# Kernel tuning notes

Hardware: AMD Instinct MI355X
Metric: run time of the kernel (lower is better)

## Reference

```python
import jax, jax.numpy as jnp
import numpy as np

EPS = 1e-5

def rms_norm(x, scale, eps=EPS):
    rms = jax.lax.rsqrt(jnp.mean(x * x, axis=-1, keepdims=True) + eps)
    return scale * (x * rms)

def act_quant(x, min_scale=0.001, max_scale=1000.0):
    # int8 activation quantization (STE in torch; fwd math only here)
    max_val = jnp.max(jnp.abs(x), axis=-1, keepdims=True)
    s = jnp.clip(127.0 / (max_val + 1e-5), min_scale, max_scale)
    return jnp.clip(jnp.round(s * x), -128.0, 127.0) / s

def weight_quant(w, num_bits=8):
    qmax = 2.0 ** (num_bits - 1) - 1.0
    scale = qmax / (jnp.max(jnp.abs(w)) + 1e-5)
    return jnp.round(jnp.clip(w * scale, -(qmax + 1.0), qmax)) / scale

def ternarize(w):
    sf = jnp.clip(1.0 / (jnp.mean(jnp.abs(w)) + 1e-5), 1e-4, 1e4)
    return jnp.sign(w * sf)

def setup_inputs() -> dict:
    key = jax.random.key(0)
    ks = jax.random.split(key, 5)
    B, S, E, H = 8, 512, 2048, 2048
    x = jax.random.normal(ks[0], (B, S, E), dtype=jnp.float32)
    # ternary {-1,0,1} init as in ternary_initialize
    def tern_init(k, shape):
        r = jax.random.uniform(k, shape, dtype=jnp.float32)
        return jnp.where(r < 1.0 / 3.0, -1.0, jnp.where(r > 2.0 / 3.0, 1.0, 0.0))
    return {
        "x": x,
        "rms_scale": jnp.ones((H,), jnp.float32),
        "W_f": tern_init(ks[1], (E, H)),
        "W_c": tern_init(ks[2], (E, H)),
        "W_g": tern_init(ks[3], (H, E)),
        "b_f": jnp.ones((H,), jnp.float32),
        "b_c": jnp.zeros((H,), jnp.float32),
        "b_g": jnp.zeros((H,), jnp.float32),
    }

def reference(x, rms_scale, W_f, W_c, W_g, b_f, b_c, b_g):
    B, S, E = x.shape
    H = W_f.shape[1]
    # quantize + ternarize weights once (identical every timestep)
    Wt_f = ternarize(weight_quant(W_f))
    Wt_c = ternarize(weight_quant(W_c))
    Wt_g = ternarize(weight_quant(W_g))  # (H, E) but E == H

    def step(h, x_t):
        xq = act_quant(rms_norm(x_t, rms_scale))
        # matmul-free linear: x @ (pos_mask - neg_mask) == x @ sign(W)
        f_t = jax.nn.sigmoid(xq @ Wt_f + b_f)
        c_t = jax.nn.silu(xq @ Wt_c + b_c)
        g_t = jax.nn.sigmoid(xq @ Wt_g + b_g)
        h_new = f_t * h + (1.0 - f_t) * c_t
        o_t = g_t * h_new
        # layer-level copy gate: sigmoid(W_g @ x_t^T)^T = sigmoid(x_t @ W_g^T), raw weights
        cg = jax.nn.sigmoid(x_t @ W_g.T)
        h_out = cg * x_t + (1.0 - cg) * h_new
        return h_out, o_t

    h0 = jnp.zeros((B, H), x.dtype)
    _, outs = jax.lax.scan(step, h0, jnp.swapaxes(x, 0, 1))  # scan over S
    return jnp.swapaxes(outs, 0, 1)  # (B, S, H)
```

## Files before the change

kernel.cpp:

```cpp
#include <hip/hip_runtime.h>
#include <hip/hip_bf16.h>
#include <cstdint>
#include <cstddef>

#define RTOT 4096
#define DIM  2048
#define NCAT 6144
#define NCHUNK 16
#define TCHUNK 32

typedef __attribute__((ext_vector_type(4))) int int4v;

__device__ __forceinline__ float fast_sigmoid(float z) {
    return __builtin_amdgcn_rcpf(1.0f + __expf(-z));
}
__device__ __forceinline__ unsigned short f2h(float f) {
    union { _Float16 h; unsigned short u; } v; v.h = (_Float16)f; return v.u;
}
__device__ __forceinline__ float h2f(unsigned short u) {
    union { _Float16 h; unsigned short u; } v; v.u = u; return (float)v.h;
}

#define GLDS(gp, lp) __builtin_amdgcn_global_load_lds( \
    (__attribute__((address_space(1))) const void*)(gp), \
    (__attribute__((address_space(3))) void*)(lp), 16, 0, 0)

__device__ __forceinline__ int4v frag_ld(const signed char* lds, int R, int lq) {
    return *(const int4v*)(lds + R * 64 + ((lq ^ ((R >> 1) & 3)) * 16));
}

__global__ __launch_bounds__(256) void prep_all(
    const float* __restrict__ x, const float* __restrict__ scale,
    const float* __restrict__ Wf, const float* __restrict__ Wc,
    const float* __restrict__ Wg,
    signed char* __restrict__ WcatT, signed char* __restrict__ Wgb,
    signed char* __restrict__ Xq, signed char* __restrict__ Q1,
    signed char* __restrict__ Q2, float* __restrict__ s_arr,
    float* __restrict__ s1_arr)
{
    __shared__ __align__(16) char smem[4224];
    int bid = blockIdx.x;
    int tid = threadIdx.x;
    if (bid < 3072) {
        signed char (*tile)[65] = (signed char(*)[65])smem;
        int j0 = (bid % 96) * 64;
        int k0 = (bid / 96) * 64;
        const float* W = (j0 < 2048) ? Wf : (j0 < 4096) ? Wc : Wg;
        int jb = j0 & 2047;
        int c  = tid & 63;
        int rr = tid >> 6;
#pragma unroll
        for (int p = 0; p < 16; ++p) {
            int kl = p * 4 + rr;
            tile[kl][c] = (signed char)(int)W[(size_t)(k0 + kl) * DIM + jb + c];
        }
        __syncthreads();
#pragma unroll
        for (int p = 0; p < 16; ++p) {
            int jl = p * 4 + rr;
            WcatT[(size_t)(j0 + jl) * DIM + k0 + c] = tile[c][jl];
        }
    } else if (bid < 4096) {
        int idx = (bid - 3072) * 4096 + tid * 16;
#pragma unroll
        for (int p = 0; p < 4; ++p) {
            float4 v = *(const float4*)(Wg + idx + p * 4);
            char4 o;
            o.x = (signed char)(int)v.x; o.y = (signed char)(int)v.y;
            o.z = (signed char)(int)v.z; o.w = (signed char)(int)v.w;
            *(char4*)(Wgb + idx + p * 4) = o;
        }
    } else {
        float* red = (float*)smem;
        float* tot = (float*)(smem + 64);
        int row = bid - 4096;
        const float* xr = x + (size_t)row * DIM + tid * 8;
        const float* sr = scale + tid * 8;
        float4 a0 = *(const float4*)(xr);
        float4 a1 = *(const float4*)(xr + 4);
        float4 c0 = *(const float4*)(sr);
        float4 c1 = *(const float4*)(sr + 4);
        float xs[8] = {a0.x, a0.y, a0.z, a0.w, a1.x, a1.y, a1.z, a1.w};
        float sc[8] = {c0.x, c0.y, c0.z, c0.w, c1.x, c1.y, c1.z, c1.w};
        float sum = 0.f, mx2 = 0.f;
#pragma unroll
        for (int i = 0; i < 8; ++i) {
            sum += xs[i] * xs[i];
            mx2 = fmaxf(mx2, fabsf(xs[i]));
        }
#pragma unroll
        for (int off = 32; off > 0; off >>= 1) {
            sum += __shfl_down(sum, off);
            mx2 = fmaxf(mx2, __shfl_down(mx2, off));
        }
        int lane = tid & 63, wv = tid >> 6;
        if (lane == 0) { red[wv] = sum; red[4 + wv] = mx2; }
        __syncthreads();
        if (tid == 0) {
            tot[0] = red[0] + red[1] + red[2] + red[3];
            tot[1] = fmaxf(fmaxf(red[4], red[5]), fmaxf(red[6], red[7]));
        }
        __syncthreads();
        float rms = 1.0f / sqrtf(tot[0] * (1.0f / 2048.0f) + 1e-5f);
        float y[8]; float mx = 0.f;
#pragma unroll
        for (int i = 0; i < 8; ++i) {
            y[i] = (xs[i] * rms) * sc[i];
            mx = fmaxf(mx, fabsf(y[i]));
        }
#pragma unroll
        for (int off = 32; off > 0; off >>= 1) mx = fmaxf(mx, __shfl_down(mx, off));
        if (lane == 0) red[8 + wv] = mx;
        __syncthreads();
        if (tid == 0)
            tot[2] = fmaxf(fmaxf(red[8], red[9]), fmaxf(red[10], red[11]));
        __syncthreads();
        float s = 127.0f / (tot[2] + 1e-5f);
        s = fminf(fmaxf(s, 0.001f), 1000.0f);
        float s1 = 127.0f / (tot[1] + 1e-5f);
        float inv_s1 = 1.0f / s1;
        if (tid == 0) { s_arr[row] = s; s1_arr[row] = s1; }
        signed char q8[8], q1b[8], q2b[8];
#pragma unroll
        for (int i = 0; i < 8; ++i) {
            float q = fminf(fmaxf(rintf(s * y[i]), -128.f), 127.f);
            q8[i] = (signed char)(int)q;
            float qq1 = fminf(fmaxf(rintf(s1 * xs[i]), -128.f), 127.f);
            q1b[i] = (signed char)(int)qq1;
            float r = xs[i] - qq1 * inv_s1;
            float qq2 = fminf(fmaxf(rintf(s1 * 256.f * r), -128.f), 127.f);
            q2b[i] = (signed char)(int)qq2;
        }
        size_t o = (size_t)row * DIM + tid * 8;
        *(int2*)(Xq + o) = *(int2*)q8;
        *(int2*)(Q1 + o) = *(int2*)q1b;
        *(int2*)(Q2 + o) = *(int2*)q2b;
    }
}

__global__ __launch_bounds__(256) void gemm_all(
    const signed char* __restrict__ Xq, const signed char* __restrict__ WcatT,
    const signed char* __restrict__ Q1, const signed char* __restrict__ Q2,
    const signed char* __restrict__ Wgb,
    const float* __restrict__ s_arr, const float* __restrict__ s1_arr,
    const float* __restrict__ b_f, const float* __restrict__ b_c,
    const float* __restrict__ b_g,
    unsigned short* __restrict__ FCG,
    unsigned short* __restrict__ U,
    unsigned short* __restrict__ V)
{
    __shared__ __align__(16) signed char lds[32768];
    int bid = blockIdx.x;
    int grp = bid / 5, r5 = bid % 5;
    int tid = threadIdx.x;
    int lane = tid & 63, wv = tid >> 6;
    int lr = lane & 15, lq = lane >> 4;
    int rA = lane >> 2;
    int gch = ((lane & 3) ^ ((lane >> 3) & 3)) * 16;

    if (r5 < 3) {
        int fb = grp * 3 + r5;
        int m0 = (fb / 48) * 128;
        int n0 = (fb % 48) * 128;
        int wm = (wv >> 1) * 64, wn = (wv & 1) * 64;
        const signed char* Ab = Xq + (size_t)m0 * DIM;
        const signed char* Bb = WcatT + (size_t)n0 * DIM;

        int4v acc[4][4] = {};
#pragma unroll
        for (int it = 0; it < 2; ++it) {
            int region = wv + it * 4;
            int rr = region * 16 + rA;
            GLDS(Ab + (size_t)rr * DIM + gch, lds + region * 1024);
            GLDS(Bb + (size_t)rr * DIM + gch, lds + 8192 + region * 1024);
        }
        for (int k6 = 0; k6 < 32; ++k6) {
            signed char* cur = lds + (k6 & 1) * 16384;
            signed char* nxt = lds + ((k6 + 1) & 1) * 16384;
            __syncthreads();
            if (k6 + 1 < 32) {
                int kt = (k6 + 1) * 64;
#pragma unroll
                for (int it = 0; it < 2; ++it) {
                    int region = wv + it * 4;
                    int rr = region * 16 + rA;
                    GLDS(Ab + (size_t)rr * DIM + kt + gch, nxt + region * 1024);
                    GLDS(Bb + (size_t)rr * DIM + kt + gch, nxt + 8192 + region * 1024);
                }
            }
            int4v af[4], bb[4];
#pragma unroll
            for (int i = 0; i < 4; ++i) af[i] = frag_ld(cur, wm + i * 16 + lr, lq);
#pragma unroll
            for (int j = 0; j < 4; ++j) bb[j] = frag_ld(cur + 8192, wn + j * 16 + lr, lq);
#pragma unroll
            for (int i = 0; i < 4; ++i)
#pragma unroll
                for (int j = 0; j < 4; ++j)
                    acc[i][j] = __builtin_amdgcn_mfma_i32_16x16x64_i8(
                        af[i], bb[j], acc[i][j], 0, 0, 0);
        }
#pragma unroll
        for (int i = 0; i < 4; ++i) {
            float rinv[4];
#pragma unroll
            for (int r = 0; r < 4; ++r)
                rinv[r] = __builtin_amdgcn_rcpf(s_arr[m0 + wm + i * 16 + lq * 4 + r]);
#pragma unroll
            for (int j = 0; j < 4; ++j) {
                int gcol = n0 + wn + j * 16 + lr;
                int sec = gcol >> 11;
                int jj = gcol & 2047;
                float bias = (sec == 0) ? b_f[jj] : (sec == 1) ? b_c[jj] : b_g[jj];
#pragma unroll
                for (int r = 0; r < 4; ++r) {
                    int grow = m0 + wm + i * 16 + lq * 4 + r;
                    float z = fmaf((float)acc[i][j][r], rinv[r], bias);
                    float sg = fast_sigmoid(z);
                    FCG[(size_t)grow * NCAT + gcol] = f2h((sec == 1) ? z * sg : sg);
                }
            }
        }
    } else {
        int cb = grp * 2 + (r5 - 3);
        int m0 = (cb >> 4) * 64;
        int n0 = (cb & 15) * 128;
        int wm = (wv >> 1) * 32, wn = (wv & 1) * 64;
        const signed char* A1b = Q1 + (size_t)m0 * DIM;
        const signed char* A2b = Q2 + (size_t)m0 * DIM;
        const signed char* Bb  = Wgb + (size_t)n0 * DIM;
        int r1 = wv * 16 + rA;

        int4v acc1[2][4] = {};
        int4v acc2[2][4] = {};
        {
            GLDS(A1b + (size_t)r1 * DIM + gch, lds + wv * 1024);
            GLDS(A2b + (size_t)r1 * DIM + gch, lds + 4096 + wv * 1024);
#pragma unroll
            for (int it = 0; it < 2; ++it) {
                int region = wv + it * 4;
                int rr = region * 16 + rA;
                GLDS(Bb + (size_t)rr * DIM + gch, lds + 8192 + region * 1024);
            }
        }
        for (int k6 = 0; k6 < 32; ++k6) {
            signed char* cur = lds + (k6 & 1) * 16384;
            signed char* nxt = lds + ((k6 + 1) & 1) * 16384;
            __syncthreads();
            if (k6 + 1 < 32) {
                int kt = (k6 + 1) * 64;
                GLDS(A1b + (size_t)r1 * DIM + kt + gch, nxt + wv * 1024);
                GLDS(A2b + (size_t)r1 * DIM + kt + gch, nxt + 4096 + wv * 1024);
#pragma unroll
                for (int it = 0; it < 2; ++it) {
                    int region = wv + it * 4;
                    int rr = region * 16 + rA;
                    GLDS(Bb + (size_t)rr * DIM + kt + gch, nxt + 8192 + region * 1024);
                }
            }
            int4v bb[4];
#pragma unroll
            for (int j = 0; j < 4; ++j) bb[j] = frag_ld(cur + 8192, wn + j * 16 + lr, lq);
#pragma unroll
            for (int i = 0; i < 2; ++i) {
                int4v a1 = frag_ld(cur, wm + i * 16 + lr, lq);
                int4v a2 = frag_ld(cur + 4096, wm + i * 16 + lr, lq);
#pragma unroll
                for (int j = 0; j < 4; ++j) {
                    acc1[i][j] = __builtin_amdgcn_mfma_i32_16x16x64_i8(
                        a1, bb[j], acc1[i][j], 0, 0, 0);
                    acc2[i][j] = __builtin_amdgcn_mfma_i32_16x16x64_i8(
                        a2, bb[j], acc2[i][j], 0, 0, 0);
                }
            }
        }
#pragma unroll
        for (int i = 0; i < 2; ++i) {
            float rinv[4];
#pragma unroll
            for (int r = 0; r < 4; ++r)
                rinv[r] = __builtin_amdgcn_rcpf(s1_arr[m0 + wm + i * 16 + lq * 4 + r]);
#pragma unroll
            for (int j = 0; j < 4; ++j) {
                int gcol = n0 + wn + j * 16 + lr;
#pragma unroll
                for (int r = 0; r < 4; ++r) {
                    int grow = m0 + wm + i * 16 + lq * 4 + r;
                    size_t go = (size_t)grow * DIM + gcol;
                    float zs = (float)acc1[i][j][r] + (float)acc2[i][j][r] * (1.f / 256.f);
                    float cg = fast_sigmoid(zs * rinv[r]);
                    float xv = ((float)Q1[go] + (float)Q2[go] * (1.f / 256.f)) * rinv[r];
                    U[go] = f2h(cg * xv);
                    V[go] = f2h(1.f - cg);
                }
            }
        }
    }
}

__global__ __launch_bounds__(256) void scan_partial(
    const unsigned short* __restrict__ FCG, const unsigned short* __restrict__ U,
    const unsigned short* __restrict__ V, float4* __restrict__ PQ4)
{
    int tp = blockIdx.x * 256 + threadIdx.x;
    int c = blockIdx.y;
    int b = blockIdx.z;
    int h0 = tp * 2;
    size_t r0 = (size_t)(b * 512 + c * TCHUNK);
    const unsigned short* fp = FCG + r0 * NCAT + h0;
    const unsigned short* up = U + r0 * DIM + h0;
    const unsigned short* vp = V + r0 * DIM + h0;
    float P0 = 1.f, Q0 = 0.f, P1 = 1.f, Q1v = 0.f;
#pragma unroll 4
    for (int t = 0; t < TCHUNK; ++t) {
        unsigned fw = *(const unsigned*)(fp);
        unsigned cw = *(const unsigned*)(fp + 2048);
        unsigned uw = *(const unsigned*)(up);
        unsigned vw = *(const unsigned*)(vp);
        float f0 = h2f(fw & 0xffff), f1 = h2f(fw >> 16);
        float c0 = h2f(cw & 0xffff), c1 = h2f(cw >> 16);
        float u0 = h2f(uw & 0xffff), u1 = h2f(uw >> 16);
        float v0 = h2f(vw & 0xffff), v1 = h2f(vw >> 16);
        float A0 = v0 * f0, A1 = v1 * f1;
        float B0 = fmaf(v0 * (1.f - f0), c0, u0);
        float B1 = fmaf(v1 * (1.f - f1), c1, u1);
        P0 = A0 * P0; Q0 = fmaf(A0, Q0, B0);
        P1 = A1 * P1; Q1v = fmaf(A1, Q1v, B1);
        fp += NCAT; up += DIM; vp += DIM;
    }
    float4 o; o.x = P0; o.y = Q0; o.z = P1; o.w = Q1v;
    PQ4[(size_t)c * 8192 + b * 1024 + tp] = o;
}

__global__ __launch_bounds__(256) void scan_final(
    const unsigned short* __restrict__ FCG, const unsigned short* __restrict__ U,
    const unsigned short* __restrict__ V, const float4* __restrict__ PQ4,
    float* __restrict__ out)
{
    int tp = blockIdx.x * 256 + threadIdx.x;
    int c = blockIdx.y;
    int b = blockIdx.z;
    int h0 = tp * 2;
    float h0s = 0.f, h1s = 0.f;
    for (int cc = 0; cc < c; ++cc) {
        float4 pq = PQ4[(size_t)cc * 8192 + b * 1024 + tp];
        h0s = fmaf(pq.x, h0s, pq.y);
        h1s = fmaf(pq.z, h1s, pq.w);
    }
    size_t r0 = (size_t)(b * 512 + c * TCHUNK);
    const unsigned short* fp = FCG + r0 * NCAT + h0;
    const unsigned short* up = U + r0 * DIM + h0;
    const unsigned short* vp = V + r0 * DIM + h0;
    float* op = out + r0 * DIM + h0;
#pragma unroll 4
    for (int t = 0; t < TCHUNK; ++t) {
        unsigned fw = *(const unsigned*)(fp);
        unsigned cw = *(const unsigned*)(fp + 2048);
        unsigned gw = *(const unsigned*)(fp + 4096);
        unsigned uw = *(const unsigned*)(up);
        unsigned vw = *(const unsigned*)(vp);
        float f0 = h2f(fw & 0xffff), f1 = h2f(fw >> 16);
        float c0 = h2f(cw & 0xffff), c1 = h2f(cw >> 16);
        float g0 = h2f(gw & 0xffff), g1 = h2f(gw >> 16);
        float u0 = h2f(uw & 0xffff), u1 = h2f(uw >> 16);
        float v0 = h2f(vw & 0xffff), v1 = h2f(vw >> 16);
        float hn0 = f0 * h0s + (1.f - f0) * c0;
        float hn1 = f1 * h1s + (1.f - f1) * c1;
        float2 ov; ov.x = g0 * hn0; ov.y = g1 * hn1;
        *(float2*)op = ov;
        h0s = fmaf(v0, hn0, u0);
        h1s = fmaf(v1, hn1, u1);
        fp += NCAT; up += DIM; vp += DIM; op += DIM;
    }
}

extern "C" void kernel_launch(void* const* d_in, const int* in_sizes, int n_in,
                              void* d_out, int out_size, void* d_ws, size_t ws_size,
                              hipStream_t stream) {
    const float* x     = (const float*)d_in[0];
    const float* rmssc = (const float*)d_in[1];
    const float* W_f   = (const float*)d_in[2];
    const float* W_c   = (const float*)d_in[3];
    const float* W_g   = (const float*)d_in[4];
    const float* b_f   = (const float*)d_in[5];
    const float* b_c   = (const float*)d_in[6];
    const float* b_g   = (const float*)d_in[7];
    float* out = (float*)d_out;

    char* ws = (char*)d_ws;
    size_t off = 0;
    auto alloc = [&](size_t bytes) -> void* {
        void* p = ws + off;
        off += (bytes + 255) & ~(size_t)255;
        return p;
    };
    signed char* WcatT = (signed char*)alloc((size_t)NCAT * DIM);
    signed char* Wgb   = (signed char*)alloc((size_t)DIM * DIM);
    signed char* Xq    = (signed char*)alloc((size_t)RTOT * DIM);
    signed char* Q1    = (signed char*)alloc((size_t)RTOT * DIM);
    signed char* Q2    = (signed char*)alloc((size_t)RTOT * DIM);
    float* s_arr       = (float*)alloc((size_t)RTOT * 4);
    float* s1_arr      = (float*)alloc((size_t)RTOT * 4);
    unsigned short* FCG = (unsigned short*)alloc((size_t)RTOT * NCAT * 2);
    unsigned short* U   = (unsigned short*)alloc((size_t)RTOT * DIM * 2);
    unsigned short* V   = (unsigned short*)alloc((size_t)RTOT * DIM * 2);
    float4* PQ4        = (float4*)alloc((size_t)NCHUNK * 8192 * 16);

    hipLaunchKernelGGL(prep_all, dim3(8192), dim3(256), 0, stream,
                       x, rmssc, W_f, W_c, W_g, WcatT, Wgb, Xq, Q1, Q2,
                       s_arr, s1_arr);
    hipLaunchKernelGGL(gemm_all, dim3(2560), dim3(256), 0, stream,
                       Xq, WcatT, Q1, Q2, Wgb, s_arr, s1_arr,
                       b_f, b_c, b_g, FCG, U, V);
    hipLaunchKernelGGL(scan_partial, dim3(DIM / 512, NCHUNK, 8), dim3(256), 0, stream,
                       FCG, U, V, PQ4);
    hipLaunchKernelGGL(scan_final, dim3(DIM / 512, NCHUNK, 8), dim3(256), 0, stream,
                       FCG, U, V, PQ4, out);
}
```

Before: 297.3 us.

## Split GEMMs and precompute scan coefficients in the f/c/g GEMM epilogue

Splits the combined GEMM into a copy-gate GEMM that writes packed (u,v) pairs and an f/c/g GEMM whose three waves each compute one gate for the same 64x64 tile. The f/c/g epilogue exchanges the gate values through LDS and emits precomputed scan coefficients (A,B) and output coefficients (g*f, g*(1-f)*c). The scans then read one or two packed words per step instead of five fp16 streams, and chunks are halved to 16 steps with 32 chunks. This cuts scan memory traffic and FCG intermediate size. In exchange the GEMM runs with 192 threads, adds an extra kernel launch, and scan_final's serial prefix over PQ4 gets longer.

```diff
diff --git a/kernel.cpp b/kernel.cpp
--- a/kernel.cpp
+++ b/kernel.cpp
@@ -6,8 +6,8 @@
 #define RTOT 4096
 #define DIM  2048
 #define NCAT 6144
-#define NCHUNK 16
-#define TCHUNK 32
+#define NCHUNK 32
+#define TCHUNK 16
 
 typedef __attribute__((ext_vector_type(4))) int int4v;
 
@@ -19,6 +19,9 @@
 }
 __device__ __forceinline__ float h2f(unsigned short u) {
     union { _Float16 h; unsigned short u; } v; v.u = u; return (float)v.h;
+}
+__device__ __forceinline__ unsigned pack2(float a, float b) {
+    return (unsigned)f2h(a) | ((unsigned)f2h(b) << 16);
 }
 
 #define GLDS(gp, lp) __builtin_amdgcn_global_load_lds( \
@@ -138,209 +141,206 @@
     }
 }
 
-__global__ __launch_bounds__(256) void gemm_all(
+__global__ __launch_bounds__(256) void gemm_cg(
+    const signed char* __restrict__ Q1, const signed char* __restrict__ Q2,
+    const signed char* __restrict__ Wgb, const float* __restrict__ s1_arr,
+    unsigned* __restrict__ UV)
+{
+    __shared__ __align__(16) signed char lds[32768];
+    int cb = blockIdx.x;
+    int m0 = (cb >> 4) * 64;
+    int n0 = (cb & 15) * 128;
+    int tid = threadIdx.x;
+    int lane = tid & 63, wv = tid >> 6;
+    int wm = (wv >> 1) * 32, wn = (wv & 1) * 64;
+    int lr = lane & 15, lq = lane >> 4;
+    int rA = lane >> 2;
+    int gch = ((lane & 3) ^ ((lane >> 3) & 3)) * 16;
+    const signed char* A1b = Q1 + (size_t)m0 * DIM;
+    const signed char* A2b = Q2 + (size_t)m0 * DIM;
+    const signed char* Bb  = Wgb + (size_t)n0 * DIM;
+    int r1 = wv * 16 + rA;
+
+    int4v acc1[2][4] = {};
+    int4v acc2[2][4] = {};
+    {
+        GLDS(A1b + (size_t)r1 * DIM + gch, lds + wv * 1024);
+        GLDS(A2b + (size_t)r1 * DIM + gch, lds + 4096 + wv * 1024);
+#pragma unroll
+        for (int it = 0; it < 2; ++it) {
+            int region = wv + it * 4;
+            GLDS(Bb + (size_t)(region * 16 + rA) * DIM + gch,
+                 lds + 8192 + region * 1024);
+        }
+    }
+    for (int k6 = 0; k6 < 32; ++k6) {
+        const signed char* cur = lds + (k6 & 1) * 16384;
+        signed char* nxt = lds + ((k6 + 1) & 1) * 16384;
+        __syncthreads();
+        if (k6 + 1 < 32) {
+            int kt = (k6 + 1) * 64;
+            GLDS(A1b + (size_t)r1 * DIM + kt + gch, nxt + wv * 1024);
+            GLDS(A2b + (size_t)r1 * DIM + kt + gch, nxt + 4096 + wv * 1024);
+#pragma unroll
+            for (int it = 0; it < 2; ++it) {
+                int region = wv + it * 4;
+                GLDS(Bb + (size_t)(region * 16 + rA) * DIM + kt + gch,
+                     nxt + 8192 + region * 1024);
+            }
+        }
+        int4v bb[4];
+#pragma unroll
+        for (int j = 0; j < 4; ++j) bb[j] = frag_ld(cur + 8192, wn + j * 16 + lr, lq);
+#pragma unroll
+        for (int i = 0; i < 2; ++i) {
+            int4v a1 = frag_ld(cur, wm + i * 16 + lr, lq);
+            int4v a2 = frag_ld(cur + 4096, wm + i * 16 + lr, lq);
+#pragma unroll
+            for (int j = 0; j < 4; ++j) {
+                acc1[i][j] = __builtin_amdgcn_mfma_i32_16x16x64_i8(
+                    a1, bb[j], acc1[i][j], 0, 0, 0);
+                acc2[i][j] = __builtin_amdgcn_mfma_i32_16x16x64_i8(
+                    a2, bb[j], acc2[i][j], 0, 0, 0);
+            }
+        }
+    }
+#pragma unroll
+    for (int i = 0; i < 2; ++i) {
+        float rinv[4];
+#pragma unroll
+        for (int r = 0; r < 4; ++r)
+            rinv[r] = __builtin_amdgcn_rcpf(s1_arr[m0 + wm + i * 16 + lq * 4 + r]);
+#pragma unroll
+        for (int j = 0; j < 4; ++j) {
+            int gcol = n0 + wn + j * 16 + lr;
+#pragma unroll
+            for (int r = 0; r < 4; ++r) {
+                int grow = m0 + wm + i * 16 + lq * 4 + r;
+                size_t go = (size_t)grow * DIM + gcol;
+                float zs = (float)acc1[i][j][r] + (float)acc2[i][j][r] * (1.f / 256.f);
+                float cg = fast_sigmoid(zs * rinv[r]);
+                float xv = ((float)Q1[go] + (float)Q2[go] * (1.f / 256.f)) * rinv[r];
+                UV[go] = pack2(cg * xv, 1.f - cg);
+            }
+        }
+    }
+}
+
+__global__ __launch_bounds__(192) void gemm_fcg3(
     const signed char* __restrict__ Xq, const signed char* __restrict__ WcatT,
-    const signed char* __restrict__ Q1, const signed char* __restrict__ Q2,
-    const signed char* __restrict__ Wgb,
-    const float* __restrict__ s_arr, const float* __restrict__ s1_arr,
+    const float* __restrict__ s_arr,
     const float* __restrict__ b_f, const float* __restrict__ b_c,
-    const float* __restrict__ b_g,
-    unsigned short* __restrict__ FCG,
-    unsigned short* __restrict__ U,
-    unsigned short* __restrict__ V)
+    const float* __restrict__ b_g, const unsigned* __restrict__ UV,
+    unsigned* __restrict__ SC, unsigned* __restrict__ SG)
 {
     __shared__ __align__(16) signed char lds[32768];
     int bid = blockIdx.x;
-    int grp = bid / 5, r5 = bid % 5;
+    int m0 = (bid >> 5) * 64;
+    int n0 = (bid & 31) * 64;
     int tid = threadIdx.x;
     int lane = tid & 63, wv = tid >> 6;
     int lr = lane & 15, lq = lane >> 4;
     int rA = lane >> 2;
     int gch = ((lane & 3) ^ ((lane >> 3) & 3)) * 16;
 
-    if (r5 < 3) {
-        int fb = grp * 3 + r5;
-        int m0 = (fb / 48) * 128;
-        int n0 = (fb % 48) * 128;
-        int wm = (wv >> 1) * 64, wn = (wv & 1) * 64;
-        const signed char* Ab = Xq + (size_t)m0 * DIM;
-        const signed char* Bb = WcatT + (size_t)n0 * DIM;
-
-        int4v acc[4][4] = {};
-#pragma unroll
-        for (int it = 0; it < 2; ++it) {
-            int region = wv + it * 4;
-            int rr = region * 16 + rA;
-            GLDS(Ab + (size_t)rr * DIM + gch, lds + region * 1024);
-            GLDS(Bb + (size_t)rr * DIM + gch, lds + 8192 + region * 1024);
-        }
-        for (int k6 = 0; k6 < 32; ++k6) {
-            signed char* cur = lds + (k6 & 1) * 16384;
-            signed char* nxt = lds + ((k6 + 1) & 1) * 16384;
-            __syncthreads();
-            if (k6 + 1 < 32) {
-                int kt = (k6 + 1) * 64;
-#pragma unroll
-                for (int it = 0; it < 2; ++it) {
-                    int region = wv + it * 4;
-                    int rr = region * 16 + rA;
-                    GLDS(Ab + (size_t)rr * DIM + kt + gch, nxt + region * 1024);
-                    GLDS(Bb + (size_t)rr * DIM + kt + gch, nxt + 8192 + region * 1024);
-                }
+    int4v acc[4][4] = {};
+    for (int r = wv; r < 16; r += 3) {
+        const signed char* g = (r < 4)
+            ? Xq + (size_t)(m0 + r * 16 + rA) * DIM
+            : WcatT + (size_t)(((r - 4) >> 2) * 2048 + n0 + ((r - 4) & 3) * 16 + rA) * DIM;
+        GLDS(g + gch, lds + r * 1024);
+    }
+    for (int k6 = 0; k6 < 32; ++k6) {
+        const signed char* cur = lds + (k6 & 1) * 16384;
+        signed char* nxt = lds + ((k6 + 1) & 1) * 16384;
+        __syncthreads();
+        if (k6 + 1 < 32) {
+            int kt = (k6 + 1) * 64;
+            for (int r = wv; r < 16; r += 3) {
+                const signed char* g = (r < 4)
+                    ? Xq + (size_t)(m0 + r * 16 + rA) * DIM
+                    : WcatT + (size_t)(((r - 4) >> 2) * 2048 + n0 + ((r - 4) & 3) * 16 + rA) * DIM;
+                GLDS(g + kt + gch, nxt + r * 1024);
             }
-            int4v af[4], bb[4];
-#pragma unroll
-            for (int i = 0; i < 4; ++i) af[i] = frag_ld(cur, wm + i * 16 + lr, lq);
-#pragma unroll
-            for (int j = 0; j < 4; ++j) bb[j] = frag_ld(cur + 8192, wn + j * 16 + lr, lq);
-#pragma unroll
-            for (int i = 0; i < 4; ++i)
-#pragma unroll
-                for (int j = 0; j < 4; ++j)
-                    acc[i][j] = __builtin_amdgcn_mfma_i32_16x16x64_i8(
-                        af[i], bb[j], acc[i][j], 0, 0, 0);
-        }
-#pragma unroll
-        for (int i = 0; i < 4; ++i) {
-            float rinv[4];
-#pragma unroll
-            for (int r = 0; r < 4; ++r)
-                rinv[r] = __builtin_amdgcn_rcpf(s_arr[m0 + wm + i * 16 + lq * 4 + r]);
-#pragma unroll
-            for (int j = 0; j < 4; ++j) {
-                int gcol = n0 + wn + j * 16 + lr;
-                int sec = gcol >> 11;
-                int jj = gcol & 2047;
-                float bias = (sec == 0) ? b_f[jj] : (sec == 1) ? b_c[jj] : b_g[jj];
-#pragma unroll
-                for (int r = 0; r < 4; ++r) {
-                    int grow = m0 + wm + i * 16 + lq * 4 + r;
-                    float z = fmaf((float)acc[i][j][r], rinv[r], bias);
-                    float sg = fast_sigmoid(z);
-                    FCG[(size_t)grow * NCAT + gcol] = f2h((sec == 1) ? z * sg : sg);
-                }
+        }
+        const signed char* Bsec = cur + 4096 + wv * 4096;
+        int4v af[4], bb[4];
+#pragma unroll
+        for (int i = 0; i < 4; ++i) af[i] = frag_ld(cur, i * 16 + lr, lq);
+#pragma unroll
+        for (int j = 0; j < 4; ++j) bb[j] = frag_ld(Bsec, j * 16 + lr, lq);
+#pragma unroll
+        for (int i = 0; i < 4; ++i)
+#pragma unroll
+            for (int j = 0; j < 4; ++j)
+                acc[i][j] = __builtin_amdgcn_mfma_i32_16x16x64_i8(
+                    af[i], bb[j], acc[i][j], 0, 0, 0);
+    }
+    __syncthreads();
+    unsigned short* ex = (unsigned short*)lds;
+    const float* bsel = (wv == 0) ? b_f : (wv == 1) ? b_c : b_g;
+#pragma unroll
+    for (int i = 0; i < 4; ++i) {
+        float rinv[4];
+#pragma unroll
+        for (int r = 0; r < 4; ++r)
+            rinv[r] = __builtin_amdgcn_rcpf(s_arr[m0 + i * 16 + lq * 4 + r]);
+#pragma unroll
+        for (int j = 0; j < 4; ++j) {
+            int hl = j * 16 + lr;
+            float bias = bsel[n0 + hl];
+#pragma unroll
+            for (int r = 0; r < 4; ++r) {
+                int tl = i * 16 + lq * 4 + r;
+                float z = fmaf((float)acc[i][j][r], rinv[r], bias);
+                float sg = fast_sigmoid(z);
+                ex[wv * 4096 + tl * 64 + hl] = f2h((wv == 1) ? z * sg : sg);
             }
         }
-    } else {
-        int cb = grp * 2 + (r5 - 3);
-        int m0 = (cb >> 4) * 64;
-        int n0 = (cb & 15) * 128;
-        int wm = (wv >> 1) * 32, wn = (wv & 1) * 64;
-        const signed char* A1b = Q1 + (size_t)m0 * DIM;
-        const signed char* A2b = Q2 + (size_t)m0 * DIM;
-        const signed char* Bb  = Wgb + (size_t)n0 * DIM;
-        int r1 = wv * 16 + rA;
-
-        int4v acc1[2][4] = {};
-        int4v acc2[2][4] = {};
-        {
-            GLDS(A1b + (size_t)r1 * DIM + gch, lds + wv * 1024);
-            GLDS(A2b + (size_t)r1 * DIM + gch, lds + 4096 + wv * 1024);
-#pragma unroll
-            for (int it = 0; it < 2; ++it) {
-                int region = wv + it * 4;
-                int rr = region * 16 + rA;
-                GLDS(Bb + (size_t)rr * DIM + gch, lds + 8192 + region * 1024);
-            }
-        }
-        for (int k6 = 0; k6 < 32; ++k6) {
-            signed char* cur = lds + (k6 & 1) * 16384;
-            signed char* nxt = lds + ((k6 + 1) & 1) * 16384;
-            __syncthreads();
-            if (k6 + 1 < 32) {
-                int kt = (k6 + 1) * 64;
-                GLDS(A1b + (size_t)r1 * DIM + kt + gch, nxt + wv * 1024);
-                GLDS(A2b + (size_t)r1 * DIM + kt + gch, nxt + 4096 + wv * 1024);
-#pragma unroll
-                for (int it = 0; it < 2; ++it) {
-                    int region = wv + it * 4;
-                    int rr = region * 16 + rA;
-                    GLDS(Bb + (size_t)rr * DIM + kt + gch, nxt + 8192 + region * 1024);
-                }
-            }
-            int4v bb[4];
-#pragma unroll
-            for (int j = 0; j < 4; ++j) bb[j] = frag_ld(cur + 8192, wn + j * 16 + lr, lq);
-#pragma unroll
-            for (int i = 0; i < 2; ++i) {
-                int4v a1 = frag_ld(cur, wm + i * 16 + lr, lq);
-                int4v a2 = frag_ld(cur + 4096, wm + i * 16 + lr, lq);
-#pragma unroll
-                for (int j = 0; j < 4; ++j) {
-                    acc1[i][j] = __builtin_amdgcn_mfma_i32_16x16x64_i8(
-                        a1, bb[j], acc1[i][j], 0, 0, 0);
-                    acc2[i][j] = __builtin_amdgcn_mfma_i32_16x16x64_i8(
-                        a2, bb[j], acc2[i][j], 0, 0, 0);
-                }
-            }
-        }
-#pragma unroll
-        for (int i = 0; i < 2; ++i) {
-            float rinv[4];
-#pragma unroll
-            for (int r = 0; r < 4; ++r)
-                rinv[r] = __builtin_amdgcn_rcpf(s1_arr[m0 + wm + i * 16 + lq * 4 + r]);
-#pragma unroll
-            for (int j = 0; j < 4; ++j) {
-                int gcol = n0 + wn + j * 16 + lr;
-#pragma unroll
-                for (int r = 0; r < 4; ++r) {
-                    int grow = m0 + wm + i * 16 + lq * 4 + r;
-                    size_t go = (size_t)grow * DIM + gcol;
-                    float zs = (float)acc1[i][j][r] + (float)acc2[i][j][r] * (1.f / 256.f);
-                    float cg = fast_sigmoid(zs * rinv[r]);
-                    float xv = ((float)Q1[go] + (float)Q2[go] * (1.f / 256.f)) * rinv[r];
-                    U[go] = f2h(cg * xv);
-                    V[go] = f2h(1.f - cg);
-                }
-            }
-        }
+    }
+    __syncthreads();
+    for (int idx = tid; idx < 4096; idx += 192) {
+        int tl = idx >> 6, hl = idx & 63;
+        float f = h2f(ex[tl * 64 + hl]);
+        float c = h2f(ex[4096 + tl * 64 + hl]);
+        float g = h2f(ex[8192 + tl * 64 + hl]);
+        size_t go = (size_t)(m0 + tl) * DIM + n0 + hl;
+        unsigned uv = UV[go];
+        float u = h2f(uv & 0xffff), v = h2f(uv >> 16);
+        float w = (1.f - f) * c;
+        SC[go] = pack2(v * f, fmaf(v, w, u));
+        SG[go] = pack2(g * f, g * w);
     }
 }
 
 __global__ __launch_bounds__(256) void scan_partial(
-    const unsigned short* __restrict__ FCG, const unsigned short* __restrict__ U,
-    const unsigned short* __restrict__ V, float4* __restrict__ PQ4)
+    const unsigned* __restrict__ SC, float4* __restrict__ PQ4)
 {
     int tp = blockIdx.x * 256 + threadIdx.x;
     int c = blockIdx.y;
     int b = blockIdx.z;
-    int h0 = tp * 2;
     size_t r0 = (size_t)(b * 512 + c * TCHUNK);
-    const unsigned short* fp = FCG + r0 * NCAT + h0;
-    const unsigned short* up = U + r0 * DIM + h0;
-    const unsigned short* vp = V + r0 * DIM + h0;
+    const uint2* scp = (const uint2*)(SC + r0 * DIM) + tp;
     float P0 = 1.f, Q0 = 0.f, P1 = 1.f, Q1v = 0.f;
-#pragma unroll 4
+#pragma unroll
     for (int t = 0; t < TCHUNK; ++t) {
-        unsigned fw = *(const unsigned*)(fp);
-        unsigned cw = *(const unsigned*)(fp + 2048);
-        unsigned uw = *(const unsigned*)(up);
-        unsigned vw = *(const unsigned*)(vp);
-        float f0 = h2f(fw & 0xffff), f1 = h2f(fw >> 16);
-        float c0 = h2f(cw & 0xffff), c1 = h2f(cw >> 16);
-        float u0 = h2f(uw & 0xffff), u1 = h2f(uw >> 16);
-        float v0 = h2f(vw & 0xffff), v1 = h2f(vw >> 16);
-        float A0 = v0 * f0, A1 = v1 * f1;
-        float B0 = fmaf(v0 * (1.f - f0), c0, u0);
-        float B1 = fmaf(v1 * (1.f - f1), c1, u1);
+        uint2 w = scp[t * (DIM / 2)];
+        float A0 = h2f(w.x & 0xffff), B0 = h2f(w.x >> 16);
+        float A1 = h2f(w.y & 0xffff), B1 = h2f(w.y >> 16);
         P0 = A0 * P0; Q0 = fmaf(A0, Q0, B0);
         P1 = A1 * P1; Q1v = fmaf(A1, Q1v, B1);
-        fp += NCAT; up += DIM; vp += DIM;
     }
     float4 o; o.x = P0; o.y = Q0; o.z = P1; o.w = Q1v;
     PQ4[(size_t)c * 8192 + b * 1024 + tp] = o;
 }
 
 __global__ __launch_bounds__(256) void scan_final(
-    const unsigned short* __restrict__ FCG, const unsigned short* __restrict__ U,
-    const unsigned short* __restrict__ V, const float4* __restrict__ PQ4,
-    float* __restrict__ out)
+    const unsigned* __restrict__ SC, const unsigned* __restrict__ SG,
+    const float4* __restrict__ PQ4, float* __restrict__ out)
 {
     int tp = blockIdx.x * 256 + threadIdx.x;
     int c = blockIdx.y;
     int b = blockIdx.z;
-    int h0 = tp * 2;
     float h0s = 0.f, h1s = 0.f;
     for (int cc = 0; cc < c; ++cc) {
         float4 pq = PQ4[(size_t)cc * 8192 + b * 1024 + tp];
@@ -348,29 +348,23 @@
         h1s = fmaf(pq.z, h1s, pq.w);
     }
     size_t r0 = (size_t)(b * 512 + c * TCHUNK);
-    const unsigned short* fp = FCG + r0 * NCAT + h0;
-    const unsigned short* up = U + r0 * DIM + h0;
-    const unsigned short* vp = V + r0 * DIM + h0;
-    float* op = out + r0 * DIM + h0;
-#pragma unroll 4
+    const uint2* scp = (const uint2*)(SC + r0 * DIM) + tp;
+    const uint2* sgp = (const uint2*)(SG + r0 * DIM) + tp;
+    float* op = out + r0 * DIM + tp * 2;
+#pragma unroll
     for (int t = 0; t < TCHUNK; ++t) {
-        unsigned fw = *(const unsigned*)(fp);
-        unsigned cw = *(const unsigned*)(fp + 2048);
-        unsigned gw = *(const unsigned*)(fp + 4096);
-        unsigned uw = *(const unsigned*)(up);
-        unsigned vw = *(const unsigned*)(vp);
-        float f0 = h2f(fw & 0xffff), f1 = h2f(fw >> 16);
-        float c0 = h2f(cw & 0xffff), c1 = h2f(cw >> 16);
-        float g0 = h2f(gw & 0xffff), g1 = h2f(gw >> 16);
-        float u0 = h2f(uw & 0xffff), u1 = h2f(uw >> 16);
-        float v0 = h2f(vw & 0xffff), v1 = h2f(vw >> 16);
-        float hn0 = f0 * h0s + (1.f - f0) * c0;
-        float hn1 = f1 * h1s + (1.f - f1) * c1;
-        float2 ov; ov.x = g0 * hn0; ov.y = g1 * hn1;
-        *(float2*)op = ov;
-        h0s = fmaf(v0, hn0, u0);
-        h1s = fmaf(v1, hn1, u1);
-        fp += NCAT; up += DIM; vp += DIM; op += DIM;
+        uint2 ws = scp[t * (DIM / 2)];
+        uint2 wg = sgp[t * (DIM / 2)];
+        float A0 = h2f(ws.x & 0xffff), B0 = h2f(ws.x >> 16);
+        float A1 = h2f(ws.y & 0xffff), B1 = h2f(ws.y >> 16);
+        float Gf0 = h2f(wg.x & 0xffff), Gw0 = h2f(wg.x >> 16);
+        float Gf1 = h2f(wg.y & 0xffff), Gw1 = h2f(wg.y >> 16);
+        float2 ov;
+        ov.x = fmaf(Gf0, h0s, Gw0);
+        ov.y = fmaf(Gf1, h1s, Gw1);
+        *(float2*)(op + (size_t)t * DIM) = ov;
+        h0s = fmaf(A0, h0s, B0);
+        h1s = fmaf(A1, h1s, B1);
     }
 }
 
@@ -401,19 +395,20 @@
     signed char* Q2    = (signed char*)alloc((size_t)RTOT * DIM);
     float* s_arr       = (float*)alloc((size_t)RTOT * 4);
     float* s1_arr      = (float*)alloc((size_t)RTOT * 4);
-    unsigned short* FCG = (unsigned short*)alloc((size_t)RTOT * NCAT * 2);
-    unsigned short* U   = (unsigned short*)alloc((size_t)RTOT * DIM * 2);
-    unsigned short* V   = (unsigned short*)alloc((size_t)RTOT * DIM * 2);
+    unsigned* UV       = (unsigned*)alloc((size_t)RTOT * DIM * 4);
+    unsigned* SC       = (unsigned*)alloc((size_t)RTOT * DIM * 4);
+    unsigned* SG       = (unsigned*)alloc((size_t)RTOT * DIM * 4);
     float4* PQ4        = (float4*)alloc((size_t)NCHUNK * 8192 * 16);
 
     hipLaunchKernelGGL(prep_all, dim3(8192), dim3(256), 0, stream,
                        x, rmssc, W_f, W_c, W_g, WcatT, Wgb, Xq, Q1, Q2,
                        s_arr, s1_arr);
-    hipLaunchKernelGGL(gemm_all, dim3(2560), dim3(256), 0, stream,
-                       Xq, WcatT, Q1, Q2, Wgb, s_arr, s1_arr,
-                       b_f, b_c, b_g, FCG, U, V);
-    hipLaunchKernelGGL(scan_partial, dim3(DIM / 512, NCHUNK, 8), dim3(256), 0, stream,
-                       FCG, U, V, PQ4);
-    hipLaunchKernelGGL(scan_final, dim3(DIM / 512, NCHUNK, 8), dim3(256), 0, stream,
-                       FCG, U, V, PQ4, out);
-}
+    hipLaunchKernelGGL(gemm_cg, dim3(1024), dim3(256), 0, stream,
+                       Q1, Q2, Wgb, s1_arr, UV);
+    hipLaunchKernelGGL(gemm_fcg3, dim3(2048), dim3(192), 0, stream,
+                       Xq, WcatT, s_arr, b_f, b_c, b_g, UV, SC, SG);
+    hipLaunchKernelGGL(scan_partial, dim3(4, NCHUNK, 8), dim3(256), 0, stream,
+                       SC, PQ4);
+    hipLaunchKernelGGL(scan_final, dim3(4, NCHUNK, 8), dim3(256), 0, stream,
+                       SC, SG, PQ4, out);
+}
```

After: 328.2 us. 10.4% more time.
